# Kernel optimization log

Hardware: AMD Instinct MI355X
Metric: run time of the kernel (lower is better)

Reference implementation:

```python
import jax, jax.numpy as jnp
import numpy as np

N = 100000   # nodes
E = 1200000  # edges
D = 64       # in_channels == out_channels, heads=1
NEG_SLOPE = 0.2  # PyG GATv2Conv default negative_slope


def setup_inputs() -> dict:
    key = jax.random.key(0)
    k1, k2, k3, k4 = jax.random.split(key, 4)
    x = jax.random.normal(k1, (N, D), dtype=jnp.float32)
    edge_index = jax.random.randint(k2, (2, E), 0, N, dtype=jnp.int32)
    # glorot-ish scale for shared linear (share_weights=True -> lin_l == lin_r)
    W = jax.random.normal(k3, (D, D), dtype=jnp.float32) * (1.0 / np.sqrt(D))
    b = jnp.zeros((D,), dtype=jnp.float32)
    att = jax.random.normal(k4, (D,), dtype=jnp.float32) * (1.0 / np.sqrt(D))
    return {"x": x, "edge_index": edge_index, "W": W, "b": b, "att": att}


def reference(x, edge_index, W, b, att):
    src = edge_index[0]  # source j (messages flow j -> i)
    dst = edge_index[1]  # target i
    # shared linear transform (share_weights=True)
    z = x @ W.T + b                                   # [N, D]
    # GATv2 score: att . leakyrelu(z_j + z_i)
    e = jax.nn.leaky_relu(z[src] + z[dst], NEG_SLOPE) @ att  # [E]
    # segment softmax over incoming edges of each target node
    m = jax.ops.segment_max(e, dst, num_segments=N)   # [N]
    ex = jnp.exp(e - m[dst])                          # [E]
    s = jax.ops.segment_sum(ex, dst, num_segments=N)  # [N]
    alpha = ex / s[dst]                               # [E]
    # SimpleConv(aggr='sum') with edge_weight=alpha on ORIGINAL x
    out = jax.ops.segment_sum(alpha[:, None] * x[src], dst, num_segments=N)  # [N, D]
    return out
```

## Files before the change

### kernel.cpp

```cpp
#include <hip/hip_runtime.h>

#define D 64
#define LOG2E 1.4426950408889634f

#define HEPT_H 32
#define SEPT 32
#define BSH 7
#define BSZ 128

using frag_ab = __attribute__((ext_vector_type(8))) short;
using f32x4   = __attribute__((ext_vector_type(4))) float;

__device__ __forceinline__ unsigned short f2bf(float f) {
    unsigned int bits = __float_as_uint(f);
    return (unsigned short)((bits + 0x7fffu + ((bits >> 16) & 1u)) >> 16);
}

__device__ __forceinline__ frag_ab pack8(float4 a, float4 b) {
    frag_ab f;
    f[0] = (short)f2bf(a.x); f[1] = (short)f2bf(a.y);
    f[2] = (short)f2bf(a.z); f[3] = (short)f2bf(a.w);
    f[4] = (short)f2bf(b.x); f[5] = (short)f2bf(b.y);
    f[6] = (short)f2bf(b.z); f[7] = (short)f2bf(b.w);
    return f;
}

__global__ __launch_bounds__(256) void gemm_z_hist(const float* __restrict__ x,
                                                   const float* __restrict__ W,
                                                   const float* __restrict__ b,
                                                   unsigned int* __restrict__ zxb,
                                                   int n,
                                                   const int* __restrict__ dst,
                                                   int* __restrict__ hist2d,
                                                   int e_cnt, int histBlk,
                                                   int nb, int nblk) {
    __shared__ float xs[64 * 68];
    int tid = threadIdx.x;

    if ((int)blockIdx.x < histBlk) {
        int* cnt = (int*)xs;
        for (int i = tid; i < nb; i += 256) cnt[i] = 0;
        __syncthreads();
        int base = blockIdx.x * (256 * HEPT_H);
        for (int j = 0; j < HEPT_H; ++j) {
            int e = base + j * 256 + tid;
            if (e < e_cnt) atomicAdd(&cnt[dst[e] >> BSH], 1);
        }
        __syncthreads();
        for (int i = tid; i < nb; i += 256)
            hist2d[(size_t)i * nblk + blockIdx.x] = cnt[i];
        return;
    }

    int row0 = (blockIdx.x - histBlk) * 64;
    for (int i = tid; i < 64 * 16; i += 256) {
        int r = i >> 4;
        int gr = row0 + r;
        float4 v = (gr < n) ? ((const float4*)x)[(size_t)gr * 16 + (i & 15)]
                            : make_float4(0.f, 0.f, 0.f, 0.f);
        *(float4*)&xs[r * 68 + (i & 15) * 4] = v;
    }

    int l  = tid & 63;
    int w  = tid >> 6;
    int lr = l & 15;
    int hi = l >> 4;
    int lk = hi * 8;

    frag_ab bfr[4][2];
#pragma unroll
    for (int colt = 0; colt < 4; ++colt) {
#pragma unroll
        for (int ks = 0; ks < 2; ++ks) {
            const float* wp = W + (colt * 16 + lr) * 64 + ks * 32 + lk;
            bfr[colt][ks] = pack8(*(const float4*)wp, *(const float4*)(wp + 4));
        }
    }

    __syncthreads();

    frag_ab afr[2];
#pragma unroll
    for (int ks = 0; ks < 2; ++ks) {
        const float* ap = &xs[(w * 16 + lr) * 68 + ks * 32 + lk];
        afr[ks] = pack8(*(const float4*)ap, *(const float4*)(ap + 4));
    }

    f32x4 zero = {0.f, 0.f, 0.f, 0.f};
    f32x4 acc[4] = {zero, zero, zero, zero};
#pragma unroll
    for (int ks = 0; ks < 2; ++ks) {
#pragma unroll
        for (int colt = 0; colt < 4; ++colt) {
            acc[colt] = __builtin_amdgcn_mfma_f32_16x16x32_bf16(
                afr[ks], bfr[colt][ks], acc[colt], 0, 0, 0);
        }
    }

#pragma unroll
    for (int colt = 0; colt < 4; ++colt) {
        int col = colt * 16 + lr;
        float bb = b[col];
#pragma unroll
        for (int r = 0; r < 4; ++r) {
            int lrow = w * 16 + hi * 4 + r;
            int row  = row0 + lrow;
            if (row < n) {
                float z  = acc[colt][r] + bb;
                float xv = xs[lrow * 68 + col];
                unsigned int u = (unsigned int)f2bf(z) |
                                 ((unsigned int)f2bf(xv) << 16);
                zxb[(size_t)row * 64 + col] = u;
            }
        }
    }
}

__global__ __launch_bounds__(256) void scan_part(const int* __restrict__ data,
                                                 int* __restrict__ part, int n) {
    __shared__ int red[256];
    int t = threadIdx.x;
    int i = blockIdx.x * 256 + t;
    red[t] = (i < n) ? data[i] : 0;
    __syncthreads();
    for (int off = 128; off >= 1; off >>= 1) {
        if (t < off) red[t] += red[t + off];
        __syncthreads();
    }
    if (t == 0) part[blockIdx.x] = red[0];
}

__global__ __launch_bounds__(512) void scan_top(int* __restrict__ part, int B) {
    __shared__ int s[512];
    int t = threadIdx.x;
    int v = (t < B) ? part[t] : 0;
    s[t] = v;
    __syncthreads();
    for (int off = 1; off < 512; off <<= 1) {
        int u = (t >= off) ? s[t - off] : 0;
        __syncthreads();
        s[t] += u;
        __syncthreads();
    }
    if (t < B) part[t] = s[t] - v;
}

__global__ __launch_bounds__(256) void scan_final_ip(int* data,
                                                     const int* __restrict__ part, int n) {
    __shared__ int s[256];
    int t = threadIdx.x;
    int i = blockIdx.x * 256 + t;
    int v = (i < n) ? data[i] : 0;
    s[t] = v;
    __syncthreads();
    for (int off = 1; off < 256; off <<= 1) {
        int u = (t >= off) ? s[t - off] : 0;
        __syncthreads();
        s[t] += u;
        __syncthreads();
    }
    int incl = s[t] + part[blockIdx.x];
    if (i < n) data[i] = incl - v;
    if (i == n - 1) data[n] = incl;
}

__global__ __launch_bounds__(256) void msd_scatter(const int* __restrict__ src,
                                                   const int* __restrict__ dst,
                                                   const int* __restrict__ histS,
                                                   unsigned int* __restrict__ packed,
                                                   int e_cnt, int nb, int nblk) {
    __shared__ int cnt[1024];
    int t = threadIdx.x;
    int blk = blockIdx.x;
    for (int i = t; i < nb; i += 256) cnt[i] = histS[(size_t)i * nblk + blk];
    __syncthreads();
    int base = blk * (256 * SEPT);
    for (int j = 0; j < SEPT; ++j) {
        int e = base + j * 256 + t;
        if (e < e_cnt) {
            int d = dst[e];
            int pos = atomicAdd(&cnt[d >> BSH], 1);
            packed[pos] = (unsigned int)src[e] | ((unsigned int)(d & (BSZ - 1)) << 24);
        }
    }
}

__global__ __launch_bounds__(256) void bucket_csr(const unsigned int* __restrict__ packed,
                                                  const int* __restrict__ histS,
                                                  int* __restrict__ rowstart,
                                                  int* __restrict__ srcids,
                                                  int n, int e_cnt, int nb, int nblk) {
    __shared__ int cnt[128];
    __shared__ int sc[128];
    __shared__ int cur[128];
    int t = threadIdx.x;
    int b = blockIdx.x;
    int lo = histS[(size_t)b * nblk];
    int hi = histS[(size_t)(b + 1) * nblk];
    int m = hi - lo;

    if (t < 128) cnt[t] = 0;
    __syncthreads();
    for (int i = t; i < m; i += 256)
        atomicAdd(&cnt[packed[lo + i] >> 24], 1);
    __syncthreads();
    if (t < 128) sc[t] = cnt[t];
    __syncthreads();
    for (int off = 1; off < 128; off <<= 1) {
        int u = (t < 128 && t >= off) ? sc[t - off] : 0;
        __syncthreads();
        if (t < 128) sc[t] += u;
        __syncthreads();
    }
    if (t < 128) {
        int excl = sc[t] - cnt[t];
        cur[t] = lo + excl;
        int node = (b << BSH) + t;
        if (node < n) rowstart[node] = lo + excl;
    }
    if (b == nb - 1 && t == 0) rowstart[n] = e_cnt;
    __syncthreads();
    for (int i = t; i < m; i += 256) {
        unsigned int p = packed[lo + i];
        int pos = atomicAdd(&cur[p >> 24], 1);
        srcids[pos] = (int)(p & 0xFFFFFFu);
    }
}

__global__ __launch_bounds__(256) void gather4b(const int* __restrict__ srcids,
                                                const int* __restrict__ rowstart,
                                                const unsigned int* __restrict__ zxb,
                                                const float* __restrict__ att,
                                                float* __restrict__ out, int n) {
    int lane = threadIdx.x & 63;
    int node = blockIdx.x * 4 + (threadIdx.x >> 6);
    if (node >= n) return;
    int q = lane & 15;
    int h = lane >> 4;
    int rs = rowstart[node], re = rowstart[node + 1];

    const uint4 zdv = *(const uint4*)(zxb + (size_t)node * 64 + 4 * q);
    float zd0 = __uint_as_float(zdv.x << 16);
    float zd1 = __uint_as_float(zdv.y << 16);
    float zd2 = __uint_as_float(zdv.z << 16);
    float zd3 = __uint_as_float(zdv.w << 16);
    float4 av = *(const float4*)(att + 4 * q);
    float a0 = av.x * LOG2E, a1 = av.y * LOG2E, a2 = av.z * LOG2E, a3 = av.w * LOG2E;

    float ax0 = 0.f, ax1 = 0.f, ax2 = 0.f, ax3 = 0.f, ssum = 0.f;
    int efull = rs + ((re - rs) & ~7);
    int e = rs;
    for (; e < efull; e += 8) {
        int s0 = srcids[e + h];
        int s1 = srcids[e + 4 + h];
        const uint4 r0 = *(const uint4*)(zxb + (size_t)s0 * 64 + 4 * q);
        const uint4 r1 = *(const uint4*)(zxb + (size_t)s1 * 64 + 4 * q);

        float v0 = __uint_as_float(r0.x << 16) + zd0; v0 = fmaxf(v0, 0.2f * v0);
        float v1 = __uint_as_float(r0.y << 16) + zd1; v1 = fmaxf(v1, 0.2f * v1);
        float v2 = __uint_as_float(r0.z << 16) + zd2; v2 = fmaxf(v2, 0.2f * v2);
        float v3 = __uint_as_float(r0.w << 16) + zd3; v3 = fmaxf(v3, 0.2f * v3);
        float p0 = v0 * a0 + v1 * a1 + v2 * a2 + v3 * a3;

        float u0 = __uint_as_float(r1.x << 16) + zd0; u0 = fmaxf(u0, 0.2f * u0);
        float u1 = __uint_as_float(r1.y << 16) + zd1; u1 = fmaxf(u1, 0.2f * u1);
        float u2 = __uint_as_float(r1.z << 16) + zd2; u2 = fmaxf(u2, 0.2f * u2);
        float u3 = __uint_as_float(r1.w << 16) + zd3; u3 = fmaxf(u3, 0.2f * u3);
        float p1 = u0 * a0 + u1 * a1 + u2 * a2 + u3 * a3;

#pragma unroll
        for (int off = 8; off >= 1; off >>= 1) {
            p0 += __shfl_xor(p0, off, 64);
            p1 += __shfl_xor(p1, off, 64);
        }
        float ex0 = __builtin_exp2f(p0);
        float ex1 = __builtin_exp2f(p1);
        ssum += ex0 + ex1;
        ax0 += ex0 * __uint_as_float(r0.x & 0xffff0000u)
             + ex1 * __uint_as_float(r1.x & 0xffff0000u);
        ax1 += ex0 * __uint_as_float(r0.y & 0xffff0000u)
             + ex1 * __uint_as_float(r1.y & 0xffff0000u);
        ax2 += ex0 * __uint_as_float(r0.z & 0xffff0000u)
             + ex1 * __uint_as_float(r1.z & 0xffff0000u);
        ax3 += ex0 * __uint_as_float(r0.w & 0xffff0000u)
             + ex1 * __uint_as_float(r1.w & 0xffff0000u);
    }
    if (e < re) {
        int e0i = e + h, e1i = e + 4 + h;
        bool l0 = e0i < re, l1 = e1i < re;
        int s0 = l0 ? srcids[e0i] : node;
        int s1 = l1 ? srcids[e1i] : node;
        const uint4 r0 = *(const uint4*)(zxb + (size_t)s0 * 64 + 4 * q);
        const uint4 r1 = *(const uint4*)(zxb + (size_t)s1 * 64 + 4 * q);

        float v0 = __uint_as_float(r0.x << 16) + zd0; v0 = fmaxf(v0, 0.2f * v0);
        float v1 = __uint_as_float(r0.y << 16) + zd1; v1 = fmaxf(v1, 0.2f * v1);
        float v2 = __uint_as_float(r0.z << 16) + zd2; v2 = fmaxf(v2, 0.2f * v2);
        float v3 = __uint_as_float(r0.w << 16) + zd3; v3 = fmaxf(v3, 0.2f * v3);
        float p0 = v0 * a0 + v1 * a1 + v2 * a2 + v3 * a3;

        float u0 = __uint_as_float(r1.x << 16) + zd0; u0 = fmaxf(u0, 0.2f * u0);
        float u1 = __uint_as_float(r1.y << 16) + zd1; u1 = fmaxf(u1, 0.2f * u1);
        float u2 = __uint_as_float(r1.z << 16) + zd2; u2 = fmaxf(u2, 0.2f * u2);
        float u3 = __uint_as_float(r1.w << 16) + zd3; u3 = fmaxf(u3, 0.2f * u3);
        float p1 = u0 * a0 + u1 * a1 + u2 * a2 + u3 * a3;

#pragma unroll
        for (int off = 8; off >= 1; off >>= 1) {
            p0 += __shfl_xor(p0, off, 64);
            p1 += __shfl_xor(p1, off, 64);
        }
        float ex0 = l0 ? __builtin_exp2f(p0) : 0.f;
        float ex1 = l1 ? __builtin_exp2f(p1) : 0.f;
        ssum += ex0 + ex1;
        ax0 += ex0 * __uint_as_float(r0.x & 0xffff0000u)
             + ex1 * __uint_as_float(r1.x & 0xffff0000u);
        ax1 += ex0 * __uint_as_float(r0.y & 0xffff0000u)
             + ex1 * __uint_as_float(r1.y & 0xffff0000u);
        ax2 += ex0 * __uint_as_float(r0.z & 0xffff0000u)
             + ex1 * __uint_as_float(r1.z & 0xffff0000u);
        ax3 += ex0 * __uint_as_float(r0.w & 0xffff0000u)
             + ex1 * __uint_as_float(r1.w & 0xffff0000u);
    }
    ssum += __shfl_xor(ssum, 16, 64); ssum += __shfl_xor(ssum, 32, 64);
    ax0  += __shfl_xor(ax0, 16, 64);  ax0  += __shfl_xor(ax0, 32, 64);
    ax1  += __shfl_xor(ax1, 16, 64);  ax1  += __shfl_xor(ax1, 32, 64);
    ax2  += __shfl_xor(ax2, 16, 64);  ax2  += __shfl_xor(ax2, 32, 64);
    ax3  += __shfl_xor(ax3, 16, 64);  ax3  += __shfl_xor(ax3, 32, 64);
    if (h == 0) {
        float inv = (re > rs) ? 1.f / ssum : 0.f;
        float4 o = make_float4(ax0 * inv, ax1 * inv, ax2 * inv, ax3 * inv);
        *(float4*)&out[(size_t)node * D + 4 * q] = o;
    }
}

extern "C" void kernel_launch(void* const* d_in, const int* in_sizes, int n_in,
                              void* d_out, int out_size, void* d_ws, size_t ws_size,
                              hipStream_t stream) {
    const float* x   = (const float*)d_in[0];
    const int*   ei  = (const int*)d_in[1];
    const float* W   = (const float*)d_in[2];
    const float* b   = (const float*)d_in[3];
    const float* att = (const float*)d_in[4];
    int n = in_sizes[0] / D;
    int e = in_sizes[1] / 2;
    const int* src = ei;
    const int* dst = ei + e;
    float* out = (float*)d_out;

    int gemmBlk = (n + 63) / 64;
    int nb      = (n + BSZ - 1) >> BSH;
    int histBlk = (e + 256 * HEPT_H - 1) / (256 * HEPT_H);
    int nblk    = histBlk;
    int scatBlk = (e + 256 * SEPT - 1) / (256 * SEPT);
    int NBH     = nb * nblk;
    int scanBlk = (NBH + 255) / 256;

    unsigned int* zxb = (unsigned int*)d_ws;
    int* hist2d   = (int*)(zxb + (size_t)n * 64);
    int* rowstart = hist2d + NBH + 1;
    int* srcids   = rowstart + n + 1;
    unsigned int* packed = (unsigned int*)(srcids + e);
    int* part     = (int*)(packed + e);

    gemm_z_hist<<<histBlk + gemmBlk, 256, 0, stream>>>(x, W, b, zxb, n,
                                                       dst, hist2d, e, histBlk, nb, nblk);
    scan_part<<<scanBlk, 256, 0, stream>>>(hist2d, part, NBH);
    scan_top<<<1, 512, 0, stream>>>(part, scanBlk);
    scan_final_ip<<<scanBlk, 256, 0, stream>>>(hist2d, part, NBH);
    msd_scatter<<<scatBlk, 256, 0, stream>>>(src, dst, hist2d, packed, e, nb, nblk);
    bucket_csr<<<nb, 256, 0, stream>>>(packed, hist2d, rowstart, srcids, n, e, nb, nblk);
    gather4b<<<(n + 3) / 4, 256, 0, stream>>>(srcids, rowstart, zxb, att, out, n);
}
```

Before: 197.9 us.

## Fuse bucket CSR build and gather into per-bucket LDS atomic accumulation

Removes the per-bucket CSR construction kernel and the per-node gather kernel. A single kernel now processes each 64-node bucket's packed edge list directly, keeping destination z rows in LDS and accumulating weighted messages and softmax denominators with LDS float atomics. Bucket size is halved to 64 nodes, so the scan and scatter shared arrays are enlarged to match. This drops a kernel launch and the srcids/rowstart round trip through global memory, but adds heavy LDS atomic contention and relies on the max-free softmax already used before.

```diff
diff --git a/kernel.cpp b/kernel.cpp
--- a/kernel.cpp
+++ b/kernel.cpp
@@ -5,8 +5,8 @@
 
 #define HEPT_H 32
 #define SEPT 32
-#define BSH 7
-#define BSZ 128
+#define BSH 6
+#define BSZ 64
 
 using frag_ab = __attribute__((ext_vector_type(8))) short;
 using f32x4   = __attribute__((ext_vector_type(4))) float;
@@ -130,13 +130,13 @@
     if (t == 0) part[blockIdx.x] = red[0];
 }
 
-__global__ __launch_bounds__(512) void scan_top(int* __restrict__ part, int B) {
-    __shared__ int s[512];
+__global__ __launch_bounds__(1024) void scan_top(int* __restrict__ part, int B) {
+    __shared__ int s[1024];
     int t = threadIdx.x;
     int v = (t < B) ? part[t] : 0;
     s[t] = v;
     __syncthreads();
-    for (int off = 1; off < 512; off <<= 1) {
+    for (int off = 1; off < 1024; off <<= 1) {
         int u = (t >= off) ? s[t - off] : 0;
         __syncthreads();
         s[t] += u;
@@ -169,7 +169,7 @@
                                                    const int* __restrict__ histS,
                                                    unsigned int* __restrict__ packed,
                                                    int e_cnt, int nb, int nblk) {
-    __shared__ int cnt[1024];
+    __shared__ int cnt[2048];
     int t = threadIdx.x;
     int blk = blockIdx.x;
     for (int i = t; i < nb; i += 256) cnt[i] = histS[(size_t)i * nblk + blk];
@@ -185,87 +185,66 @@
     }
 }
 
-__global__ __launch_bounds__(256) void bucket_csr(const unsigned int* __restrict__ packed,
+__global__ __launch_bounds__(256) void gather_acc(const unsigned int* __restrict__ packed,
                                                   const int* __restrict__ histS,
-                                                  int* __restrict__ rowstart,
-                                                  int* __restrict__ srcids,
-                                                  int n, int e_cnt, int nb, int nblk) {
-    __shared__ int cnt[128];
-    __shared__ int sc[128];
-    __shared__ int cur[128];
+                                                  const unsigned int* __restrict__ zxb,
+                                                  const float* __restrict__ att,
+                                                  float* __restrict__ out,
+                                                  int n, int nblk) {
+    __shared__ float zrow[BSZ * 68];
+    __shared__ float accum[BSZ * 68];
+    __shared__ float ssum[BSZ];
     int t = threadIdx.x;
     int b = blockIdx.x;
+    int node0 = b << BSH;
     int lo = histS[(size_t)b * nblk];
     int hi = histS[(size_t)(b + 1) * nblk];
-    int m = hi - lo;
-
-    if (t < 128) cnt[t] = 0;
-    __syncthreads();
-    for (int i = t; i < m; i += 256)
-        atomicAdd(&cnt[packed[lo + i] >> 24], 1);
-    __syncthreads();
-    if (t < 128) sc[t] = cnt[t];
-    __syncthreads();
-    for (int off = 1; off < 128; off <<= 1) {
-        int u = (t < 128 && t >= off) ? sc[t - off] : 0;
-        __syncthreads();
-        if (t < 128) sc[t] += u;
-        __syncthreads();
-    }
-    if (t < 128) {
-        int excl = sc[t] - cnt[t];
-        cur[t] = lo + excl;
-        int node = (b << BSH) + t;
-        if (node < n) rowstart[node] = lo + excl;
-    }
-    if (b == nb - 1 && t == 0) rowstart[n] = e_cnt;
-    __syncthreads();
-    for (int i = t; i < m; i += 256) {
-        unsigned int p = packed[lo + i];
-        int pos = atomicAdd(&cur[p >> 24], 1);
-        srcids[pos] = (int)(p & 0xFFFFFFu);
-    }
-}
-
-__global__ __launch_bounds__(256) void gather4b(const int* __restrict__ srcids,
-                                                const int* __restrict__ rowstart,
-                                                const unsigned int* __restrict__ zxb,
-                                                const float* __restrict__ att,
-                                                float* __restrict__ out, int n) {
-    int lane = threadIdx.x & 63;
-    int node = blockIdx.x * 4 + (threadIdx.x >> 6);
-    if (node >= n) return;
+
+    for (int i = t; i < BSZ * 16; i += 256) {
+        int r = i >> 4, seg = i & 15;
+        int node = node0 + r;
+        uint4 v = (node < n) ? *(const uint4*)(zxb + (size_t)node * 64 + seg * 4)
+                             : make_uint4(0u, 0u, 0u, 0u);
+        float* zp = &zrow[r * 68 + seg * 4];
+        zp[0] = __uint_as_float(v.x << 16);
+        zp[1] = __uint_as_float(v.y << 16);
+        zp[2] = __uint_as_float(v.z << 16);
+        zp[3] = __uint_as_float(v.w << 16);
+        float* ap = &accum[r * 68 + seg * 4];
+        ap[0] = 0.f; ap[1] = 0.f; ap[2] = 0.f; ap[3] = 0.f;
+    }
+    if (t < BSZ) ssum[t] = 0.f;
+    __syncthreads();
+
+    int lane = t & 63;
+    int w    = t >> 6;
     int q = lane & 15;
     int h = lane >> 4;
-    int rs = rowstart[node], re = rowstart[node + 1];
-
-    const uint4 zdv = *(const uint4*)(zxb + (size_t)node * 64 + 4 * q);
-    float zd0 = __uint_as_float(zdv.x << 16);
-    float zd1 = __uint_as_float(zdv.y << 16);
-    float zd2 = __uint_as_float(zdv.z << 16);
-    float zd3 = __uint_as_float(zdv.w << 16);
     float4 av = *(const float4*)(att + 4 * q);
     float a0 = av.x * LOG2E, a1 = av.y * LOG2E, a2 = av.z * LOG2E, a3 = av.w * LOG2E;
 
-    float ax0 = 0.f, ax1 = 0.f, ax2 = 0.f, ax3 = 0.f, ssum = 0.f;
-    int efull = rs + ((re - rs) & ~7);
-    int e = rs;
-    for (; e < efull; e += 8) {
-        int s0 = srcids[e + h];
-        int s1 = srcids[e + 4 + h];
+    for (int eb = lo + w * 8; eb < hi; eb += 32) {
+        int e0i = eb + h, e1i = eb + 4 + h;
+        bool l0 = e0i < hi, l1 = e1i < hi;
+        unsigned int pk0 = packed[l0 ? e0i : (hi - 1)];
+        unsigned int pk1 = packed[l1 ? e1i : (hi - 1)];
+        int s0 = (int)(pk0 & 0xFFFFFFu), d0 = (int)(pk0 >> 24);
+        int s1 = (int)(pk1 & 0xFFFFFFu), d1 = (int)(pk1 >> 24);
         const uint4 r0 = *(const uint4*)(zxb + (size_t)s0 * 64 + 4 * q);
         const uint4 r1 = *(const uint4*)(zxb + (size_t)s1 * 64 + 4 * q);
-
-        float v0 = __uint_as_float(r0.x << 16) + zd0; v0 = fmaxf(v0, 0.2f * v0);
-        float v1 = __uint_as_float(r0.y << 16) + zd1; v1 = fmaxf(v1, 0.2f * v1);
-        float v2 = __uint_as_float(r0.z << 16) + zd2; v2 = fmaxf(v2, 0.2f * v2);
-        float v3 = __uint_as_float(r0.w << 16) + zd3; v3 = fmaxf(v3, 0.2f * v3);
+        const float4 zd0 = *(const float4*)&zrow[d0 * 68 + 4 * q];
+        const float4 zd1 = *(const float4*)&zrow[d1 * 68 + 4 * q];
+
+        float v0 = __uint_as_float(r0.x << 16) + zd0.x; v0 = fmaxf(v0, 0.2f * v0);
+        float v1 = __uint_as_float(r0.y << 16) + zd0.y; v1 = fmaxf(v1, 0.2f * v1);
+        float v2 = __uint_as_float(r0.z << 16) + zd0.z; v2 = fmaxf(v2, 0.2f * v2);
+        float v3 = __uint_as_float(r0.w << 16) + zd0.w; v3 = fmaxf(v3, 0.2f * v3);
         float p0 = v0 * a0 + v1 * a1 + v2 * a2 + v3 * a3;
 
-        float u0 = __uint_as_float(r1.x << 16) + zd0; u0 = fmaxf(u0, 0.2f * u0);
-        float u1 = __uint_as_float(r1.y << 16) + zd1; u1 = fmaxf(u1, 0.2f * u1);
-        float u2 = __uint_as_float(r1.z << 16) + zd2; u2 = fmaxf(u2, 0.2f * u2);
-        float u3 = __uint_as_float(r1.w << 16) + zd3; u3 = fmaxf(u3, 0.2f * u3);
+        float u0 = __uint_as_float(r1.x << 16) + zd1.x; u0 = fmaxf(u0, 0.2f * u0);
+        float u1 = __uint_as_float(r1.y << 16) + zd1.y; u1 = fmaxf(u1, 0.2f * u1);
+        float u2 = __uint_as_float(r1.z << 16) + zd1.z; u2 = fmaxf(u2, 0.2f * u2);
+        float u3 = __uint_as_float(r1.w << 16) + zd1.w; u3 = fmaxf(u3, 0.2f * u3);
         float p1 = u0 * a0 + u1 * a1 + u2 * a2 + u3 * a3;
 
 #pragma unroll
@@ -273,64 +252,39 @@
             p0 += __shfl_xor(p0, off, 64);
             p1 += __shfl_xor(p1, off, 64);
         }
-        float ex0 = __builtin_exp2f(p0);
-        float ex1 = __builtin_exp2f(p1);
-        ssum += ex0 + ex1;
-        ax0 += ex0 * __uint_as_float(r0.x & 0xffff0000u)
-             + ex1 * __uint_as_float(r1.x & 0xffff0000u);
-        ax1 += ex0 * __uint_as_float(r0.y & 0xffff0000u)
-             + ex1 * __uint_as_float(r1.y & 0xffff0000u);
-        ax2 += ex0 * __uint_as_float(r0.z & 0xffff0000u)
-             + ex1 * __uint_as_float(r1.z & 0xffff0000u);
-        ax3 += ex0 * __uint_as_float(r0.w & 0xffff0000u)
-             + ex1 * __uint_as_float(r1.w & 0xffff0000u);
-    }
-    if (e < re) {
-        int e0i = e + h, e1i = e + 4 + h;
-        bool l0 = e0i < re, l1 = e1i < re;
-        int s0 = l0 ? srcids[e0i] : node;
-        int s1 = l1 ? srcids[e1i] : node;
-        const uint4 r0 = *(const uint4*)(zxb + (size_t)s0 * 64 + 4 * q);
-        const uint4 r1 = *(const uint4*)(zxb + (size_t)s1 * 64 + 4 * q);
-
-        float v0 = __uint_as_float(r0.x << 16) + zd0; v0 = fmaxf(v0, 0.2f * v0);
-        float v1 = __uint_as_float(r0.y << 16) + zd1; v1 = fmaxf(v1, 0.2f * v1);
-        float v2 = __uint_as_float(r0.z << 16) + zd2; v2 = fmaxf(v2, 0.2f * v2);
-        float v3 = __uint_as_float(r0.w << 16) + zd3; v3 = fmaxf(v3, 0.2f * v3);
-        float p0 = v0 * a0 + v1 * a1 + v2 * a2 + v3 * a3;
-
-        float u0 = __uint_as_float(r1.x << 16) + zd0; u0 = fmaxf(u0, 0.2f * u0);
-        float u1 = __uint_as_float(r1.y << 16) + zd1; u1 = fmaxf(u1, 0.2f * u1);
-        float u2 = __uint_as_float(r1.z << 16) + zd2; u2 = fmaxf(u2, 0.2f * u2);
-        float u3 = __uint_as_float(r1.w << 16) + zd3; u3 = fmaxf(u3, 0.2f * u3);
-        float p1 = u0 * a0 + u1 * a1 + u2 * a2 + u3 * a3;
-
-#pragma unroll
-        for (int off = 8; off >= 1; off >>= 1) {
-            p0 += __shfl_xor(p0, off, 64);
-            p1 += __shfl_xor(p1, off, 64);
-        }
         float ex0 = l0 ? __builtin_exp2f(p0) : 0.f;
         float ex1 = l1 ? __builtin_exp2f(p1) : 0.f;
-        ssum += ex0 + ex1;
-        ax0 += ex0 * __uint_as_float(r0.x & 0xffff0000u)
-             + ex1 * __uint_as_float(r1.x & 0xffff0000u);
-        ax1 += ex0 * __uint_as_float(r0.y & 0xffff0000u)
-             + ex1 * __uint_as_float(r1.y & 0xffff0000u);
-        ax2 += ex0 * __uint_as_float(r0.z & 0xffff0000u)
-             + ex1 * __uint_as_float(r1.z & 0xffff0000u);
-        ax3 += ex0 * __uint_as_float(r0.w & 0xffff0000u)
-             + ex1 * __uint_as_float(r1.w & 0xffff0000u);
-    }
-    ssum += __shfl_xor(ssum, 16, 64); ssum += __shfl_xor(ssum, 32, 64);
-    ax0  += __shfl_xor(ax0, 16, 64);  ax0  += __shfl_xor(ax0, 32, 64);
-    ax1  += __shfl_xor(ax1, 16, 64);  ax1  += __shfl_xor(ax1, 32, 64);
-    ax2  += __shfl_xor(ax2, 16, 64);  ax2  += __shfl_xor(ax2, 32, 64);
-    ax3  += __shfl_xor(ax3, 16, 64);  ax3  += __shfl_xor(ax3, 32, 64);
-    if (h == 0) {
-        float inv = (re > rs) ? 1.f / ssum : 0.f;
-        float4 o = make_float4(ax0 * inv, ax1 * inv, ax2 * inv, ax3 * inv);
-        *(float4*)&out[(size_t)node * D + 4 * q] = o;
+
+        float* ar0 = &accum[d0 * 68 + 4 * q];
+        atomicAdd(&ar0[0], ex0 * __uint_as_float(r0.x & 0xffff0000u));
+        atomicAdd(&ar0[1], ex0 * __uint_as_float(r0.y & 0xffff0000u));
+        atomicAdd(&ar0[2], ex0 * __uint_as_float(r0.z & 0xffff0000u));
+        atomicAdd(&ar0[3], ex0 * __uint_as_float(r0.w & 0xffff0000u));
+        float* ar1 = &accum[d1 * 68 + 4 * q];
+        atomicAdd(&ar1[0], ex1 * __uint_as_float(r1.x & 0xffff0000u));
+        atomicAdd(&ar1[1], ex1 * __uint_as_float(r1.y & 0xffff0000u));
+        atomicAdd(&ar1[2], ex1 * __uint_as_float(r1.z & 0xffff0000u));
+        atomicAdd(&ar1[3], ex1 * __uint_as_float(r1.w & 0xffff0000u));
+        if (q == 0) {
+            atomicAdd(&ssum[d0], ex0);
+            atomicAdd(&ssum[d1], ex1);
+        }
+    }
+    __syncthreads();
+    if (t < BSZ) {
+        float s = ssum[t];
+        ssum[t] = (s > 0.f) ? __builtin_amdgcn_rcpf(s) : 0.f;
+    }
+    __syncthreads();
+    for (int i = t; i < BSZ * 16; i += 256) {
+        int r = i >> 4, seg = i & 15;
+        int node = node0 + r;
+        if (node < n) {
+            float inv = ssum[r];
+            const float* ap = &accum[r * 68 + seg * 4];
+            float4 o = make_float4(ap[0] * inv, ap[1] * inv, ap[2] * inv, ap[3] * inv);
+            *(float4*)&out[(size_t)node * D + seg * 4] = o;
+        }
     }
 }
 
@@ -358,17 +312,14 @@
 
     unsigned int* zxb = (unsigned int*)d_ws;
     int* hist2d   = (int*)(zxb + (size_t)n * 64);
-    int* rowstart = hist2d + NBH + 1;
-    int* srcids   = rowstart + n + 1;
-    unsigned int* packed = (unsigned int*)(srcids + e);
+    unsigned int* packed = (unsigned int*)(hist2d + NBH + 1);
     int* part     = (int*)(packed + e);
 
     gemm_z_hist<<<histBlk + gemmBlk, 256, 0, stream>>>(x, W, b, zxb, n,
                                                        dst, hist2d, e, histBlk, nb, nblk);
     scan_part<<<scanBlk, 256, 0, stream>>>(hist2d, part, NBH);
-    scan_top<<<1, 512, 0, stream>>>(part, scanBlk);
+    scan_top<<<1, 1024, 0, stream>>>(part, scanBlk);
     scan_final_ip<<<scanBlk, 256, 0, stream>>>(hist2d, part, NBH);
     msd_scatter<<<scatBlk, 256, 0, stream>>>(src, dst, hist2d, packed, e, nb, nblk);
-    bucket_csr<<<nb, 256, 0, stream>>>(packed, hist2d, rowstart, srcids, n, e, nb, nblk);
-    gather4b<<<(n + 3) / 4, 256, 0, stream>>>(srcids, rowstart, zxb, att, out, n);
-}
+    gather_acc<<<nb, 256, 0, stream>>>(packed, hist2d, zxb, att, out, n, nblk);
+}
```

Result: slower. 607.6 us (+206.9%).
